# Kernel optimization log

Hardware: AMD Instinct MI355X
Metric: run time of the kernel (lower is better)

The kernel has to match this reference:

```python
import jax, jax.numpy as jnp
import numpy as np

B, L, T, D = 4, 256, 256, 512
NEG_INF = -1e30


def setup_inputs() -> dict:
    key = jax.random.key(0)
    ks = jax.random.split(key, 8)
    x = jax.random.normal(ks[0], (B, L, D), dtype=jnp.float32)
    memory = jax.random.normal(ks[1], (B, T, D), dtype=jnp.float32)
    memory_mask = jnp.ones((B, T), dtype=jnp.int32)
    scale = 1.0 / np.sqrt(D)
    W1 = jax.random.normal(ks[2], (D, D), dtype=jnp.float32) * scale
    b1 = jnp.zeros((D,), dtype=jnp.float32)
    W2 = jax.random.normal(ks[3], (D, D), dtype=jnp.float32) * scale
    b2 = jnp.zeros((D,), dtype=jnp.float32)
    wt = jax.random.normal(ks[4], (D,), dtype=jnp.float32) * scale
    bt = jnp.zeros((), dtype=jnp.float32)
    return {"x": x, "memory": memory, "W1": W1, "b1": b1, "W2": W2,
            "b2": b2, "wt": wt, "bt": bt, "memory_mask": memory_mask}


def reference(x, memory, W1, b1, W2, b2, wt, bt, memory_mask):
    # item1: [B,L,D], item2: [B,T,D]
    item1 = jnp.einsum('bld,ed->ble', x, W1) + b1
    item2 = jnp.einsum('btd,ed->bte', memory, W2) + b2
    # additive (Bahdanau) score: tanh of broadcast sum, then GEMV with wt -> [B,L,T]
    item = jnp.tanh(item1[:, :, None, :] + item2[:, None, :, :])  # [B,L,T,D]
    S = jnp.einsum('bltd,d->blt', item, wt) + bt
    # memory mask: [B,1,T]
    valid = (memory_mask[:, None, :] != 0)
    # direction == 'forward': keep t >= l (upper triangular incl. diagonal)
    fwd_mask = jnp.triu(jnp.ones((L, T), dtype=bool))
    S = jnp.where(valid & fwd_mask[None, :, :], S, NEG_INF)
    P = jax.nn.softmax(S, axis=-1)  # dropout p=0.0 -> identity
    return jnp.einsum('blt,btd->bld', P, memory)
```

## Files before the change

kernel.cpp:

```cpp
#include <hip/hip_runtime.h>
#include <math.h>

#define BB 4
#define LL 256
#define TT 256
#define DD 512

#define EXP2K 2.885390081777927f

using short8 = __attribute__((ext_vector_type(8))) short;
using f32x4  = __attribute__((ext_vector_type(4))) float;

__device__ __forceinline__ unsigned cvt2bf(float a, float b) {
  unsigned r;
  asm("v_cvt_pk_bf16_f32 %0, %1, %2" : "=v"(r) : "v"(a), "v"(b));
  return r;
}

__global__ __launch_bounds__(256) void proj_gemm(
    const float* __restrict__ x, const float* __restrict__ mem,
    const float* __restrict__ W1, const float* __restrict__ b1,
    const float* __restrict__ W2, const float* __restrict__ b2,
    float* __restrict__ E1, float* __restrict__ E2c)
{
  __shared__ __align__(16) char Abuf[32 * 144];
  __shared__ __align__(16) char Bbuf[64 * 144];

  const int tid = threadIdx.x;
  const int m0 = blockIdx.x * 32;
  const int n0 = blockIdx.y * 64;
  const bool second = (m0 >= BB * LL);

  const float* A    = second ? mem + (size_t)(m0 - BB * LL) * DD
                             : x   + (size_t)m0 * DD;
  const float* W    = second ? W2 : W1;
  const float* bias = second ? b2 : b1;

  const int srow = tid >> 4;
  const int kq   = (tid & 15) * 4;

  const int lane = tid & 63;
  const int wid  = tid >> 6;
  const int r0   = (wid & 1) * 16;
  const int n0w  = (wid >> 1) * 32;
  const int lr   = lane & 15;
  const int lg   = lane >> 4;

  const int aoff  = (r0 + lr) * 144 + lg * 16;
  const int boff0 = (n0w + lr) * 144 + lg * 16;
  const int boff1 = (n0w + 16 + lr) * 144 + lg * 16;

  f32x4 acc0 = {0.f, 0.f, 0.f, 0.f};
  f32x4 acc1 = {0.f, 0.f, 0.f, 0.f};

  for (int kc = 0; kc < DD; kc += 64) {
    __syncthreads();
#pragma unroll
    for (int p = 0; p < 2; ++p) {
      const int r = srow + p * 16;
      float4 v = *(const float4*)(A + (size_t)r * DD + kc + kq);
      uint2 u = {cvt2bf(v.x, v.y), cvt2bf(v.z, v.w)};
      *(uint2*)(Abuf + r * 144 + kq * 2) = u;
    }
#pragma unroll
    for (int p = 0; p < 4; ++p) {
      const int r = srow + p * 16;
      float4 v = *(const float4*)(W + (size_t)(n0 + r) * DD + kc + kq);
      uint2 u = {cvt2bf(v.x, v.y), cvt2bf(v.z, v.w)};
      *(uint2*)(Bbuf + r * 144 + kq * 2) = u;
    }
    __syncthreads();
#pragma unroll
    for (int ks = 0; ks < 2; ++ks) {
      short8 af  = *(const short8*)(Abuf + aoff  + ks * 64);
      short8 bf0 = *(const short8*)(Bbuf + boff0 + ks * 64);
      short8 bf1 = *(const short8*)(Bbuf + boff1 + ks * 64);
      acc0 = __builtin_amdgcn_mfma_f32_16x16x32_bf16(af, bf0, acc0, 0, 0, 0);
      acc1 = __builtin_amdgcn_mfma_f32_16x16x32_bf16(af, bf1, acc1, 0, 0, 0);
    }
  }

#pragma unroll
  for (int nf = 0; nf < 2; ++nf) {
    const f32x4 a = nf ? acc1 : acc0;
    const int col = n0 + n0w + nf * 16 + lr;
    const float bv = bias[col];
#pragma unroll
    for (int i = 0; i < 4; ++i) {
      const int mrow = m0 + r0 + lg * 4 + i;
      const float val = exp2f((a[i] + bv) * EXP2K);
      if (!second) {
        E1[(size_t)mrow * DD + col] = val;
      } else {
        const int m2 = mrow - BB * LL;
        E2c[((size_t)(col >> 2) * (BB * TT) + m2) * 4 + (col & 3)] = val;
      }
    }
  }
}

__global__ __launch_bounds__(512) void fused_attn(
    const float* __restrict__ E1, const float* __restrict__ E2c,
    const float* __restrict__ wt, const float* __restrict__ mem,
    const int* __restrict__ mask, float* __restrict__ out)
{
  __shared__ float prt[2][4][8][64];
  __shared__ float S[2][TT];
  __shared__ __align__(8) float Pt[TT][2];
  __shared__ float rinvS[2];

  const int tid = threadIdx.x;
  const int tl  = tid & 63;
  const int wv  = tid >> 6;
  const int dq  = __builtin_amdgcn_readfirstlane(wv);

  const int bid = blockIdx.x;
  const int k   = bid & 7;
  const int b   = k >> 1;
  const int lp  = (bid >> 3) + ((k & 1) << 6);

  const int r0 = lp;
  const int r1 = 255 - lp;
  const int tc0 = r0 >> 6;
  const int tc1 = r1 >> 6;

  const size_t strE2 = (size_t)(BB * TT);
  const float4* wp  = (const float4*)wt + dq * 16;
  const float4* q0p = (const float4*)(E1 + (size_t)(b * LL + r0) * DD) + dq * 16;
  const float4* q1p = (const float4*)(E1 + (size_t)(b * LL + r1) * DD) + dq * 16;

  for (int tc = tc0; tc < 4; ++tc) {
    const bool shr = (tc >= tc1);
    const int t = tc * 64 + tl;
    const float4* vp = (const float4*)E2c + (size_t)(dq * 16) * strE2 + (b * TT + t);

    float a0 = 0.f, a1 = 0.f, a2 = 0.f, a3 = 0.f;
    float b0 = 0.f, b1 = 0.f, b2 = 0.f, b3 = 0.f;
    if (shr) {
#pragma unroll 8
      for (int j = 0; j < 16; ++j) {
        float4 vv = vp[(size_t)j * strE2];
        float4 q0 = q0p[j];
        float4 q1 = q1p[j];
        float4 w  = wp[j];
        a0 = fmaf(w.x, __builtin_amdgcn_rcpf(fmaf(q0.x, vv.x, 1.0f)), a0);
        a1 = fmaf(w.y, __builtin_amdgcn_rcpf(fmaf(q0.y, vv.y, 1.0f)), a1);
        a2 = fmaf(w.z, __builtin_amdgcn_rcpf(fmaf(q0.z, vv.z, 1.0f)), a2);
        a3 = fmaf(w.w, __builtin_amdgcn_rcpf(fmaf(q0.w, vv.w, 1.0f)), a3);
        b0 = fmaf(w.x, __builtin_amdgcn_rcpf(fmaf(q1.x, vv.x, 1.0f)), b0);
        b1 = fmaf(w.y, __builtin_amdgcn_rcpf(fmaf(q1.y, vv.y, 1.0f)), b1);
        b2 = fmaf(w.z, __builtin_amdgcn_rcpf(fmaf(q1.z, vv.z, 1.0f)), b2);
        b3 = fmaf(w.w, __builtin_amdgcn_rcpf(fmaf(q1.w, vv.w, 1.0f)), b3);
      }
    } else {
#pragma unroll 8
      for (int j = 0; j < 16; ++j) {
        float4 vv = vp[(size_t)j * strE2];
        float4 q0 = q0p[j];
        float4 w  = wp[j];
        a0 = fmaf(w.x, __builtin_amdgcn_rcpf(fmaf(q0.x, vv.x, 1.0f)), a0);
        a1 = fmaf(w.y, __builtin_amdgcn_rcpf(fmaf(q0.y, vv.y, 1.0f)), a1);
        a2 = fmaf(w.z, __builtin_amdgcn_rcpf(fmaf(q0.z, vv.z, 1.0f)), a2);
        a3 = fmaf(w.w, __builtin_amdgcn_rcpf(fmaf(q0.w, vv.w, 1.0f)), a3);
      }
    }
    prt[0][tc][dq][tl] = (a0 + a1) + (a2 + a3);
    if (shr) prt[1][tc][dq][tl] = (b0 + b1) + (b2 + b3);
  }
  __syncthreads();

  {
    const int rr = tid >> 8;
    const int t  = tid & 255;
    const int lo = (rr ? tc1 : tc0) << 6;
    if (t >= lo) {
      const float* pp = &prt[rr][t >> 6][0][t & 63];
      float s = 0.f;
#pragma unroll
      for (int oc = 0; oc < 8; ++oc) s += pp[oc * 64];
      S[rr][t] = s;
    }
  }
  __syncthreads();

  if (wv < 2) {
    const int row = wv ? r1 : r0;
    const int tb = tl * 4;
    float4 h = *(const float4*)(&S[wv][tb]);
    const int4 mk = *(const int4*)(mask + b * TT + tb);
    float v0 = (tb + 0 >= row && mk.x != 0) ? -2.0f * h.x : -1e30f;
    float v1 = (tb + 1 >= row && mk.y != 0) ? -2.0f * h.y : -1e30f;
    float v2 = (tb + 2 >= row && mk.z != 0) ? -2.0f * h.z : -1e30f;
    float v3 = (tb + 3 >= row && mk.w != 0) ? -2.0f * h.w : -1e30f;
    float mx = fmaxf(fmaxf(v0, v1), fmaxf(v2, v3));
#pragma unroll
    for (int o = 1; o < 64; o <<= 1) mx = fmaxf(mx, __shfl_xor(mx, o));
    float e0 = __expf(v0 - mx), e1 = __expf(v1 - mx),
          e2 = __expf(v2 - mx), e3 = __expf(v3 - mx);
    Pt[tb + 0][wv] = e0; Pt[tb + 1][wv] = e1;
    Pt[tb + 2][wv] = e2; Pt[tb + 3][wv] = e3;
    float sm = (e0 + e1) + (e2 + e3);
#pragma unroll
    for (int o = 1; o < 64; o <<= 1) sm += __shfl_xor(sm, o);
    if (tl == 0) rinvS[wv] = 1.0f / sm;
  }
  __syncthreads();

  const int dd = tid;
  const float* mp = mem + ((size_t)b * TT) * DD + dd;
  float ax0 = 0.f, ax1 = 0.f;
#pragma unroll 4
  for (int t = r0; t < r1; ++t) {
    ax0 = fmaf(Pt[t][0], mp[(size_t)t * DD], ax0);
  }
#pragma unroll 4
  for (int t = r1; t < TT; ++t) {
    float2 p = *(const float2*)(&Pt[t][0]);
    const float mv = mp[(size_t)t * DD];
    ax0 = fmaf(p.x, mv, ax0);
    ax1 = fmaf(p.y, mv, ax1);
  }
  out[((size_t)(b * LL + r0)) * DD + dd] = ax0 * rinvS[0];
  out[((size_t)(b * LL + r1)) * DD + dd] = ax1 * rinvS[1];
}

extern "C" void kernel_launch(void* const* d_in, const int* in_sizes, int n_in,
                              void* d_out, int out_size, void* d_ws, size_t ws_size,
                              hipStream_t stream) {
  const float* x   = (const float*)d_in[0];
  const float* mem = (const float*)d_in[1];
  const float* W1  = (const float*)d_in[2];
  const float* b1  = (const float*)d_in[3];
  const float* W2  = (const float*)d_in[4];
  const float* b2  = (const float*)d_in[5];
  const float* wt  = (const float*)d_in[6];
  const int* mask  = (const int*)d_in[8];
  float* outp = (float*)d_out;

  float* E1  = (float*)d_ws;
  float* E2c = E1 + (size_t)BB * LL * DD;

  proj_gemm<<<dim3((BB * LL + BB * TT) / 32, DD / 64), 256, 0, stream>>>(
      x, mem, W1, b1, W2, b2, E1, E2c);
  fused_attn<<<512, 512, 0, stream>>>(
      E1, E2c, wt, mem, mask, outp);
}
```

Measured before the change: 39.16 us.

## Split P·V product into separate bf16 MFMA GEMM kernel

Removes the scalar fp32 P·memory accumulation from the fused attention kernel, which now writes normalized probabilities to a global workspace. A new third kernel computes P·V per batch with bf16 MFMA tiles, converting memory to bf16 transposed in shared memory. This trades the per-block scalar reduction for tensor-core GEMM throughput, at the cost of an extra launch, a global round trip for P, and bf16 precision on P and V. Masked-out columns of S get a large sentinel so the full row of P is written as zeros.

```diff
diff --git a/kernel.cpp b/kernel.cpp
--- a/kernel.cpp
+++ b/kernel.cpp
@@ -8,8 +8,8 @@
 
 #define EXP2K 2.885390081777927f
 
-using short8 = __attribute__((ext_vector_type(8))) short;
-using f32x4  = __attribute__((ext_vector_type(4))) float;
+using short8  = __attribute__((ext_vector_type(8))) short;
+using f32x4   = __attribute__((ext_vector_type(4))) float;
 
 __device__ __forceinline__ unsigned cvt2bf(float a, float b) {
   unsigned r;
@@ -99,15 +99,13 @@
   }
 }
 
-__global__ __launch_bounds__(512) void fused_attn(
+__global__ __launch_bounds__(512) void score_softmax(
     const float* __restrict__ E1, const float* __restrict__ E2c,
-    const float* __restrict__ wt, const float* __restrict__ mem,
-    const int* __restrict__ mask, float* __restrict__ out)
+    const float* __restrict__ wt, const int* __restrict__ mask,
+    float* __restrict__ Pg)
 {
   __shared__ float prt[2][4][8][64];
   __shared__ float S[2][TT];
-  __shared__ __align__(8) float Pt[TT][2];
-  __shared__ float rinvS[2];
 
   const int tid = threadIdx.x;
   const int tl  = tid & 63;
@@ -179,6 +177,8 @@
 #pragma unroll
       for (int oc = 0; oc < 8; ++oc) s += pp[oc * 64];
       S[rr][t] = s;
+    } else {
+      S[rr][t] = 5e29f;
     }
   }
   __syncthreads();
@@ -197,31 +197,93 @@
     for (int o = 1; o < 64; o <<= 1) mx = fmaxf(mx, __shfl_xor(mx, o));
     float e0 = __expf(v0 - mx), e1 = __expf(v1 - mx),
           e2 = __expf(v2 - mx), e3 = __expf(v3 - mx);
-    Pt[tb + 0][wv] = e0; Pt[tb + 1][wv] = e1;
-    Pt[tb + 2][wv] = e2; Pt[tb + 3][wv] = e3;
     float sm = (e0 + e1) + (e2 + e3);
 #pragma unroll
     for (int o = 1; o < 64; o <<= 1) sm += __shfl_xor(sm, o);
-    if (tl == 0) rinvS[wv] = 1.0f / sm;
-  }
-  __syncthreads();
-
-  const int dd = tid;
-  const float* mp = mem + ((size_t)b * TT) * DD + dd;
-  float ax0 = 0.f, ax1 = 0.f;
-#pragma unroll 4
-  for (int t = r0; t < r1; ++t) {
-    ax0 = fmaf(Pt[t][0], mp[(size_t)t * DD], ax0);
-  }
-#pragma unroll 4
-  for (int t = r1; t < TT; ++t) {
-    float2 p = *(const float2*)(&Pt[t][0]);
-    const float mv = mp[(size_t)t * DD];
-    ax0 = fmaf(p.x, mv, ax0);
-    ax1 = fmaf(p.y, mv, ax1);
-  }
-  out[((size_t)(b * LL + r0)) * DD + dd] = ax0 * rinvS[0];
-  out[((size_t)(b * LL + r1)) * DD + dd] = ax1 * rinvS[1];
+    const float rinv = 1.0f / sm;
+    float4 pv = {e0 * rinv, e1 * rinv, e2 * rinv, e3 * rinv};
+    *(float4*)(Pg + (size_t)(b * LL + row) * TT + tb) = pv;
+  }
+}
+
+__global__ __launch_bounds__(256) void pv_gemm(
+    const float* __restrict__ Pg, const float* __restrict__ mem,
+    float* __restrict__ out)
+{
+  __shared__ __align__(16) char Abuf[32 * 144];
+  __shared__ __align__(16) char Bbuf[64 * 144];
+
+  const int tid = threadIdx.x;
+  const int bid = blockIdx.x;
+  const int b   = bid >> 6;
+  const int rem = bid & 63;
+  const int m0  = (rem >> 3) * 32;
+  const int n0  = (rem & 7) * 64;
+
+  const int arow = tid >> 3;
+  const int k8   = (tid & 7) * 8;
+  const int nq   = tid & 15;
+  const int kp0  = tid >> 4;
+
+  const int lane = tid & 63;
+  const int wid  = tid >> 6;
+  const int r0   = (wid & 1) * 16;
+  const int n0w  = (wid >> 1) * 32;
+  const int lr   = lane & 15;
+  const int lg   = lane >> 4;
+
+  const int aoff  = (r0 + lr) * 144 + lg * 16;
+  const int boff0 = (n0w + lr) * 144 + lg * 16;
+  const int boff1 = (n0w + 16 + lr) * 144 + lg * 16;
+
+  f32x4 acc0 = {0.f, 0.f, 0.f, 0.f};
+  f32x4 acc1 = {0.f, 0.f, 0.f, 0.f};
+
+  const float* Pb = Pg + (size_t)(b * LL) * TT;
+  const float* Mb = mem + (size_t)(b * TT) * DD;
+
+  for (int kc = 0; kc < TT; kc += 64) {
+    __syncthreads();
+    {
+      float4 a1 = *(const float4*)(Pb + (size_t)(m0 + arow) * TT + kc + k8);
+      float4 a2 = *(const float4*)(Pb + (size_t)(m0 + arow) * TT + kc + k8 + 4);
+      uint4 u = {cvt2bf(a1.x, a1.y), cvt2bf(a1.z, a1.w),
+                 cvt2bf(a2.x, a2.y), cvt2bf(a2.z, a2.w)};
+      *(uint4*)(Abuf + arow * 144 + k8 * 2) = u;
+    }
+#pragma unroll
+    for (int ii = 0; ii < 2; ++ii) {
+      const int kpair = kp0 + ii * 16;
+      const int krow  = kc + kpair * 2;
+      const int n     = n0 + nq * 4;
+      float4 fa = *(const float4*)(Mb + (size_t)krow * DD + n);
+      float4 fb = *(const float4*)(Mb + (size_t)(krow + 1) * DD + n);
+      *(unsigned*)(Bbuf + (nq * 4 + 0) * 144 + kpair * 4) = cvt2bf(fa.x, fb.x);
+      *(unsigned*)(Bbuf + (nq * 4 + 1) * 144 + kpair * 4) = cvt2bf(fa.y, fb.y);
+      *(unsigned*)(Bbuf + (nq * 4 + 2) * 144 + kpair * 4) = cvt2bf(fa.z, fb.z);
+      *(unsigned*)(Bbuf + (nq * 4 + 3) * 144 + kpair * 4) = cvt2bf(fa.w, fb.w);
+    }
+    __syncthreads();
+#pragma unroll
+    for (int ks = 0; ks < 2; ++ks) {
+      short8 af  = *(const short8*)(Abuf + aoff  + ks * 64);
+      short8 bf0 = *(const short8*)(Bbuf + boff0 + ks * 64);
+      short8 bf1 = *(const short8*)(Bbuf + boff1 + ks * 64);
+      acc0 = __builtin_amdgcn_mfma_f32_16x16x32_bf16(af, bf0, acc0, 0, 0, 0);
+      acc1 = __builtin_amdgcn_mfma_f32_16x16x32_bf16(af, bf1, acc1, 0, 0, 0);
+    }
+  }
+
+#pragma unroll
+  for (int nf = 0; nf < 2; ++nf) {
+    const f32x4 a = nf ? acc1 : acc0;
+    const int col = n0 + n0w + nf * 16 + lr;
+#pragma unroll
+    for (int i = 0; i < 4; ++i) {
+      const int mrow = m0 + r0 + lg * 4 + i;
+      out[(size_t)(b * LL + mrow) * DD + col] = a[i];
+    }
+  }
 }
 
 extern "C" void kernel_launch(void* const* d_in, const int* in_sizes, int n_in,
@@ -239,9 +301,10 @@
 
   float* E1  = (float*)d_ws;
   float* E2c = E1 + (size_t)BB * LL * DD;
+  float* Pg  = E2c + (size_t)BB * TT * DD;
 
   proj_gemm<<<dim3((BB * LL + BB * TT) / 32, DD / 64), 256, 0, stream>>>(
       x, mem, W1, b1, W2, b2, E1, E2c);
-  fused_attn<<<512, 512, 0, stream>>>(
-      E1, E2c, wt, mem, mask, outp);
-}
+  score_softmax<<<512, 512, 0, stream>>>(E1, E2c, wt, mask, Pg);
+  pv_gemm<<<256, 256, 0, stream>>>(Pg, mem, outp);
+}
```

Measured after the change: 34.48 us. 11.9% less time.
